# Kernel tuning notes

Measured on AMD Instinct MI355X. Metric: run time of the kernel, lower is better.

Reference implementation:

```python
import jax, jax.numpy as jnp
import numpy as np

N = 50000   # nodes
E = 800000  # edges
G = 64      # graphs in batch
H1, D1 = 2, 64   # gat1: 2 heads x 64
D2 = 32          # gat2: 1 head x 32
IN = 1
EPS = 1e-5


def _gat(h, src, dst, W, al, ar, Wres, bias, Hh, D):
    # DGL GATConv (eval mode): project, per-edge attention, edge softmax over dst, scatter-sum, residual + bias
    feat = (h @ W).reshape(N, Hh, D)                     # [N,H,D]
    el = jnp.sum(feat * al, axis=-1)                     # [N,H]
    er = jnp.sum(feat * ar, axis=-1)                     # [N,H]
    e = jax.nn.leaky_relu(el[src] + er[dst], 0.2)        # [E,H]
    m = jax.ops.segment_max(e, dst, num_segments=N)      # [N,H] (stable softmax)
    a = jnp.exp(e - m[dst])
    s = jax.ops.segment_sum(a, dst, num_segments=N)
    alpha = a / s[dst]                                   # [E,H]
    msg = feat[src] * alpha[:, :, None]                  # [E,H,D]
    rst = jax.ops.segment_sum(msg, dst, num_segments=N)  # [N,H,D]
    res = (h @ Wres).reshape(N, Hh, D)
    return rst + res + bias.reshape(1, Hh, D)


def _bn(x, gamma, beta, mean, var):
    return (x - mean) * jax.lax.rsqrt(var + EPS) * gamma + beta


def setup_inputs() -> dict:
    key = jax.random.key(0)
    ks = jax.random.split(key, 32)
    rn = lambda i, shape: jax.random.normal(ks[i], shape, jnp.float32) * 0.1
    inp = {
        'feat': jax.random.normal(ks[0], (N, IN), jnp.float32),
        'W1': rn(1, (IN, H1 * D1)), 'al1': rn(2, (H1, D1)), 'ar1': rn(3, (H1, D1)),
        'res1': rn(4, (IN, H1 * D1)), 'b1': rn(5, (H1 * D1,)),
        'g1_gamma': jnp.ones((H1 * D1,), jnp.float32), 'g1_beta': jnp.zeros((H1 * D1,), jnp.float32),
        'g1_mean': rn(6, (H1 * D1,)), 'g1_var': jax.random.uniform(ks[7], (H1 * D1,), jnp.float32) + 0.5,
        'W2': rn(8, (H1 * D1, D2)), 'al2': rn(9, (1, D2)), 'ar2': rn(10, (1, D2)),
        'res2': rn(11, (H1 * D1, D2)), 'b2': rn(12, (D2,)),
        'g2_gamma': jnp.ones((D2,), jnp.float32), 'g2_beta': jnp.zeros((D2,), jnp.float32),
        'g2_mean': rn(13, (D2,)), 'g2_var': jax.random.uniform(ks[14], (D2,), jnp.float32) + 0.5,
        'Wd1': rn(15, (D2, H1 * D1)), 'bd1': rn(16, (H1 * D1,)),
        'gd_gamma': jnp.ones((H1 * D1,), jnp.float32), 'gd_beta': jnp.zeros((H1 * D1,), jnp.float32),
        'gd_mean': rn(17, (H1 * D1,)), 'gd_var': jax.random.uniform(ks[18], (H1 * D1,), jnp.float32) + 0.5,
        'Wd2': rn(19, (H1 * D1, IN)), 'bd2': rn(20, (IN,)),
        'src': jax.random.randint(ks[21], (E,), 0, N, jnp.int32),
        'dst': jax.random.randint(ks[22], (E,), 0, N, jnp.int32),
        'graph_ids': jnp.sort(jax.random.randint(ks[23], (N,), 0, G, jnp.int32)),
    }
    return inp


def reference(feat, W1, al1, ar1, res1, b1, g1_gamma, g1_beta, g1_mean, g1_var,
              W2, al2, ar2, res2, b2, g2_gamma, g2_beta, g2_mean, g2_var,
              Wd1, bd1, gd_gamma, gd_beta, gd_mean, gd_var, Wd2, bd2,
              src, dst, graph_ids):
    h = _gat(feat, src, dst, W1, al1, ar1, res1, b1, H1, D1)   # [N,2,64]
    h = h.reshape(N, H1 * D1)
    h = jax.nn.relu(_bn(h, g1_gamma, g1_beta, g1_mean, g1_var))
    h = _gat(h, src, dst, W2, al2, ar2, res2, b2, 1, D2)       # [N,1,32]
    h = h.reshape(N, D2)
    h = jax.nn.relu(_bn(h, g2_gamma, g2_beta, g2_mean, g2_var))
    # dgl.mean_nodes over batched graphs
    counts = jax.ops.segment_sum(jnp.ones((N,), h.dtype), graph_ids, num_segments=G)
    graph_rep = jax.ops.segment_sum(h, graph_ids, num_segments=G) / jnp.maximum(counts, 1.0)[:, None]
    # decoder: Linear -> BN -> ReLU -> Linear (dropout off in eval)
    d = jax.nn.relu(_bn(h @ Wd1 + bd1, gd_gamma, gd_beta, gd_mean, gd_var))
    reconstruction = d @ Wd2 + bd2
    return graph_rep, reconstruction
```

## Files before the change

kernel.cpp:

```cpp
#include <hip/hip_runtime.h>
#include <hip/hip_bf16.h>

#define NN 50000
#define NE 800000
#define NG 64
#define C1 128
#define D2 32
#define NB 196
#define BN_EPS 1e-5f

#define CST_A   0
#define CST_B   2
#define CST_P   4
#define CST_Q   132
#define CST_R   260
#define CST_SC2 388
#define CST_RC2 420
#define CST_SD  452
#define CST_RD  580
#define CST_N   1024

#define UO_DEG   0
#define UO_CNT   50000
#define ZERO_UNITS 50004
#define UO_FLAG  50004
#define UO_LOC   50008
#define UO_BSUM  100008
#define UO_CARRY 100264
#define UO_ESRC  100520
#define UO_EOFF  500520
#define UO_FCAN  900520
#define UO_CST   950520
#define UO_F2    951544
#define UO_RS2   1751544
#define UO_EL2   3351544
#define UO_ER2   3401544
#define UO_END   3451544

__device__ __forceinline__ float lrelu(float x) { return fmaxf(x, 0.2f * x); }
__device__ __forceinline__ float bu2f(unsigned int u) {
    union { unsigned int i; float f; } v; v.i = (u & 0xFFFFu) << 16; return v.f;
}
__device__ __forceinline__ unsigned short f2bu(float f) {
    union { float f; unsigned int i; } v; v.f = f;
    unsigned int r = v.i + 0x7FFFu + ((v.i >> 16) & 1u);
    return (unsigned short)(r >> 16);
}
__device__ __forceinline__ float pk_lo(unsigned int w) {
    union { unsigned int i; float f; } v; v.i = w << 16; return v.f;
}
__device__ __forceinline__ float pk_hi(unsigned int w) {
    union { unsigned int i; float f; } v; v.i = w & 0xFFFF0000u; return v.f;
}
__device__ __forceinline__ float ldw(const void* p, int i, int bf) {
    return bf ? bu2f(((const unsigned short*)p)[i]) : ((const float*)p)[i];
}
__device__ __forceinline__ int offat(const int* loc, const int* carry, int i) {
    return loc[i] + carry[i >> 8];
}
__device__ __forceinline__ int sniff64(const unsigned int* fw, int l) {
    int cnt = 0;
    for (int j = l; j < 256; j += 64) {
        unsigned int b = (fw[j] >> 8) & 0x7Fu;
        cnt += (b >= 0x3Au && b <= 0x41u) ? 1 : 0;
    }
#pragma unroll
    for (int m = 32; m >= 1; m >>= 1) cnt += __shfl_xor(cnt, m);
    return (cnt > 128) ? 1 : 0;
}

__global__ void k_prep(const void* __restrict__ feat, const int* __restrict__ dst,
                       float* __restrict__ fcan, int* __restrict__ deg,
                       unsigned short* __restrict__ eoff,
                       const void* W1, const void* al1, const void* ar1,
                       const void* res1, const void* b1,
                       const void* g1g, const void* g1b, const void* g1m, const void* g1v,
                       const void* b2v, const void* g2g, const void* g2b,
                       const void* g2m, const void* g2v,
                       const void* bd1, const void* gdg, const void* gdb,
                       const void* gdm, const void* gdv,
                       int* __restrict__ flag, float* __restrict__ cst) {
    __shared__ int sBf;
    int t = threadIdx.x;
    if (t < 64) {
        int bf = sniff64((const unsigned int*)feat, t);
        if (t == 0) sBf = bf;
    }
    __syncthreads();
    int bf = sBf;

    if (blockIdx.x == 0) {
        if (t == 0) *flag = bf;
        if (t < 128) {
            if (t < 2) {
                float a = 0.0f, b = 0.0f;
                for (int d = 0; d < 64; ++d) {
                    float w = ldw(W1, t * 64 + d, bf);
                    a += w * ldw(al1, t * 64 + d, bf);
                    b += w * ldw(ar1, t * 64 + d, bf);
                }
                cst[CST_A + t] = a;
                cst[CST_B + t] = b;
            }
            {
                float sc = rsqrtf(ldw(g1v, t, bf) + BN_EPS) * ldw(g1g, t, bf);
                cst[CST_P + t] = ldw(W1, t, bf) * sc;
                cst[CST_Q + t] = ldw(res1, t, bf) * sc;
                cst[CST_R + t] = (ldw(b1, t, bf) - ldw(g1m, t, bf)) * sc + ldw(g1b, t, bf);
            }
            if (t < D2) {
                float sc = rsqrtf(ldw(g2v, t, bf) + BN_EPS) * ldw(g2g, t, bf);
                cst[CST_SC2 + t] = sc;
                cst[CST_RC2 + t] = (ldw(b2v, t, bf) - ldw(g2m, t, bf)) * sc + ldw(g2b, t, bf);
            }
            {
                float sc = rsqrtf(ldw(gdv, t, bf) + BN_EPS) * ldw(gdg, t, bf);
                cst[CST_SD + t] = sc;
                cst[CST_RD + t] = (ldw(bd1, t, bf) - ldw(gdm, t, bf)) * sc + ldw(gdb, t, bf);
            }
        }
    }

    int k = blockIdx.x * blockDim.x + t;
    if (k < NN) fcan[k] = ldw(feat, k, bf);
    if (k < NE) eoff[k] = (unsigned short)atomicAdd(&deg[dst[k]], 1);
}

__global__ __launch_bounds__(256) void k_scanA(const int* __restrict__ deg,
                                               int* __restrict__ loc,
                                               int* __restrict__ bsum,
                                               int* __restrict__ carry,
                                               int* __restrict__ cnt) {
    __shared__ int tmp[256];
    __shared__ int isLast;
    int t = threadIdx.x;
    int i = blockIdx.x * 256 + t;
    int v = (i < NN) ? deg[i] : 0;
    tmp[t] = v;
    __syncthreads();
    for (int off = 1; off < 256; off <<= 1) {
        int u = (t >= off) ? tmp[t - off] : 0;
        __syncthreads();
        tmp[t] += u;
        __syncthreads();
    }
    if (i < NN) loc[i] = tmp[t] - v;
    if (t == 255) {
        bsum[blockIdx.x] = tmp[255];
        __threadfence();
        int old = atomicAdd(cnt, 1);
        isLast = (old == NB - 1) ? 1 : 0;
    }
    __syncthreads();
    if (isLast) {
        __threadfence();
        int bv = (t < NB) ? bsum[t] : 0;
        tmp[t] = bv;
        __syncthreads();
        for (int off = 1; off < 256; off <<= 1) {
            int u = (t >= off) ? tmp[t - off] : 0;
            __syncthreads();
            tmp[t] += u;
            __syncthreads();
        }
        carry[t] = tmp[t] - bv;
    }
}

__global__ void k_fill(const int* __restrict__ src, const int* __restrict__ dst,
                       const int* __restrict__ loc, const int* __restrict__ carry,
                       const unsigned short* __restrict__ eoff,
                       unsigned short* __restrict__ esrc) {
    int k = blockIdx.x * blockDim.x + threadIdx.x;
    if (k >= NE) return;
    int d = dst[k];
    esrc[offat(loc, carry, d) + (int)eoff[k]] = (unsigned short)src[k];
}

__global__ __launch_bounds__(256) void k_layer1(
        const float* __restrict__ fcan, const void* W2, const void* res2,
        const void* al2, const void* ar2,
        const int* __restrict__ flag, const float* __restrict__ cst,
        const int* __restrict__ loc, const int* __restrict__ carry,
        const unsigned short* __restrict__ esrc,
        unsigned short* __restrict__ F2, float* __restrict__ RS2,
        float* __restrict__ EL2, float* __restrict__ ER2) {
    __shared__ unsigned int sW2pk[32 * 66];
    __shared__ unsigned int sR2pk[32 * 66];
    __shared__ unsigned int sH1pk[32 * 66];
    __shared__ float sP[C1], sQ[C1], sR[C1];
    __shared__ float sAl[D2], sAr[D2];
    int t = threadIdx.x;
    int bf = *flag;
    for (int u = t; u < 2048; u += 256) {
        int cw = u >> 5, l2 = u & 31;
        unsigned int wlo = (unsigned int)f2bu(ldw(W2, cw * D2 + l2, bf));
        unsigned int whi = (unsigned int)f2bu(ldw(W2, (cw + 64) * D2 + l2, bf));
        sW2pk[l2 * 66 + cw] = wlo | (whi << 16);
        unsigned int rlo = (unsigned int)f2bu(ldw(res2, cw * D2 + l2, bf));
        unsigned int rhi = (unsigned int)f2bu(ldw(res2, (cw + 64) * D2 + l2, bf));
        sR2pk[l2 * 66 + cw] = rlo | (rhi << 16);
    }
    if (t < C1) { sP[t] = cst[CST_P + t]; sQ[t] = cst[CST_Q + t]; sR[t] = cst[CST_R + t]; }
    if (t < D2) { sAl[t] = ldw(al2, t, bf); sAr[t] = ldw(ar2, t, bf); }
    __syncthreads();

    int l = t & 31;
    int g = t >> 5;
    int base = blockIdx.x * 32;
    float A0 = cst[CST_A + 0], A1 = cst[CST_A + 1];
    float B0 = cst[CST_B + 0], B1 = cst[CST_B + 1];

    int e0k[4], e1k[4];
    float fiK[4];
#pragma unroll
    for (int k = 0; k < 4; ++k) {
        int i = base + g * 4 + k;
        if (i < NN) {
            e0k[k] = offat(loc, carry, i);
            e1k[k] = (i + 1 < NN) ? offat(loc, carry, i + 1) : NE;
            fiK[k] = fcan[i];
        } else { e0k[k] = 0; e1k[k] = 0; fiK[k] = 0.0f; }
    }
    float S0[4], S1[4], N0[4], N1[4];
#pragma unroll
    for (int k = 0; k < 4; ++k) { S0[k] = S1[k] = N0[k] = N1[k] = 0.0f; }
    int sA[4];
#pragma unroll
    for (int k = 0; k < 4; ++k) sA[k] = (e0k[k] + l < e1k[k]) ? (int)esrc[e0k[k] + l] : 0;
    float fA[4];
#pragma unroll
    for (int k = 0; k < 4; ++k) fA[k] = fcan[sA[k]];
#pragma unroll
    for (int k = 0; k < 4; ++k) {
        if (e0k[k] + l < e1k[k]) {
            float w0 = __expf(lrelu(A0 * fA[k] + B0 * fiK[k]));
            float w1 = __expf(lrelu(A1 * fA[k] + B1 * fiK[k]));
            S0[k] += w0; N0[k] += w0 * fA[k];
            S1[k] += w1; N1[k] += w1 * fA[k];
        }
    }
#pragma unroll
    for (int k = 0; k < 4; ++k) {
        for (int e = e0k[k] + l + 32; e < e1k[k]; e += 32) {
            int s = (int)esrc[e];
            float fs = fcan[s];
            float w0 = __expf(lrelu(A0 * fs + B0 * fiK[k]));
            float w1 = __expf(lrelu(A1 * fs + B1 * fiK[k]));
            S0[k] += w0; N0[k] += w0 * fs;
            S1[k] += w1; N1[k] += w1 * fs;
        }
    }
#pragma unroll
    for (int m = 16; m >= 1; m >>= 1) {
#pragma unroll
        for (int k = 0; k < 4; ++k) {
            S0[k] += __shfl_xor(S0[k], m); N0[k] += __shfl_xor(N0[k], m);
            S1[k] += __shfl_xor(S1[k], m); N1[k] += __shfl_xor(N1[k], m);
        }
    }
#pragma unroll
    for (int k = 0; k < 4; ++k) {
        int slot = g * 4 + k;
        float T0 = S0[k] > 0.0f ? N0[k] / S0[k] : 0.0f;
        float T1 = S1[k] > 0.0f ? N1[k] / S1[k] : 0.0f;
        float h0  = fmaxf(sP[l]      * T0 + sQ[l]      * fiK[k] + sR[l],      0.0f);
        float h1v = fmaxf(sP[l + 32] * T0 + sQ[l + 32] * fiK[k] + sR[l + 32], 0.0f);
        float h2v = fmaxf(sP[l + 64] * T1 + sQ[l + 64] * fiK[k] + sR[l + 64], 0.0f);
        float h3v = fmaxf(sP[l + 96] * T1 + sQ[l + 96] * fiK[k] + sR[l + 96], 0.0f);
        sH1pk[slot * 66 + l]      = (unsigned int)f2bu(h0)  | ((unsigned int)f2bu(h2v) << 16);
        sH1pk[slot * 66 + l + 32] = (unsigned int)f2bu(h1v) | ((unsigned int)f2bu(h3v) << 16);
    }
    __syncthreads();

    int w = t >> 6;
    int half = (t >> 5) & 1;
    int nb0 = w * 8 + half * 4;
    float aF[4] = {0.f, 0.f, 0.f, 0.f}, aR[4] = {0.f, 0.f, 0.f, 0.f};
    for (int cw = 0; cw < 64; cw += 2) {
        uint2 wq = *(const uint2*)&sW2pk[l * 66 + cw];
        uint2 rq = *(const uint2*)&sR2pk[l * 66 + cw];
        float w_a = pk_lo(wq.x), w_b = pk_hi(wq.x), w_c = pk_lo(wq.y), w_d = pk_hi(wq.y);
        float r_a = pk_lo(rq.x), r_b = pk_hi(rq.x), r_c = pk_lo(rq.y), r_d = pk_hi(rq.y);
#pragma unroll
        for (int n = 0; n < 4; ++n) {
            uint2 hq = *(const uint2*)&sH1pk[(nb0 + n) * 66 + cw];
            float h_a = pk_lo(hq.x), h_b = pk_hi(hq.x), h_c = pk_lo(hq.y), h_d = pk_hi(hq.y);
            aF[n] = fmaf(h_a, w_a, fmaf(h_b, w_b, fmaf(h_c, w_c, fmaf(h_d, w_d, aF[n]))));
            aR[n] = fmaf(h_a, r_a, fmaf(h_b, r_b, fmaf(h_c, r_c, fmaf(h_d, r_d, aR[n]))));
        }
    }
#pragma unroll
    for (int n = 0; n < 4; ++n) {
        int i = base + nb0 + n;
        if (i < NN) {
            float elp = aF[n] * sAl[l], erp = aF[n] * sAr[l];
#pragma unroll
            for (int m = 16; m >= 1; m >>= 1) {
                elp += __shfl_xor(elp, m);
                erp += __shfl_xor(erp, m);
            }
            if (l == 0) { EL2[i] = elp; ER2[i] = erp; }
            F2[(size_t)i * D2 + l]  = f2bu(aF[n]);
            RS2[(size_t)i * D2 + l] = aR[n];
        }
    }
}

__global__ __launch_bounds__(256) void k_final(
        const void* Wd1, const void* Wd2, const void* bd2,
        const int* __restrict__ flag, const float* __restrict__ cst,
        const int* __restrict__ loc, const int* __restrict__ carry,
        const unsigned short* __restrict__ esrc,
        const unsigned short* __restrict__ F2, float* __restrict__ RS2,
        const float* __restrict__ EL2, const float* __restrict__ ER2,
        float* __restrict__ out) {
    __shared__ float sWd1[C1 * D2];
    __shared__ float sWd2[C1];
    __shared__ float sSd[C1], sRd[C1];
    __shared__ float sSc2[D2], sRc2[D2];
    __shared__ float sH2[8 * D2];
    int t = threadIdx.x;
    int bf = *flag;
    for (int u = t; u < C1 * D2; u += 256) sWd1[u] = ldw(Wd1, u, bf);
    for (int u = t; u < C1; u += 256) {
        sWd2[u] = ldw(Wd2, u, bf);
        sSd[u] = cst[CST_SD + u]; sRd[u] = cst[CST_RD + u];
    }
    if (t < D2) { sSc2[t] = cst[CST_SC2 + t]; sRc2[t] = cst[CST_RC2 + t]; }
    __syncthreads();

    int i = (blockIdx.x * 256 + t) >> 5;
    int l = t & 31;
    int nb = t >> 5;

    float eri = ER2[i];
    int e0 = offat(loc, carry, i);
    int e1 = (i + 1 < NN) ? offat(loc, carry, i + 1) : NE;
    float aF0 = 0.0f, aF1 = 0.0f, aF2 = 0.0f, aF3 = 0.0f;
    float S0 = 0.0f, S1 = 0.0f, S2 = 0.0f, S3 = 0.0f;
    int e = e0;
    for (; e < e1 && (e & 3); ++e) {
        int sA = (int)esrc[e];
        float wA = __expf(lrelu(EL2[sA] + eri));
        S0 += wA;
        aF0 = fmaf(wA, bu2f(F2[(size_t)sA * D2 + l]), aF0);
    }
    for (; e + 3 < e1; e += 4) {
        ushort4 q = *(const ushort4*)&esrc[e];
        int sA = q.x, sB = q.y, sC = q.z, sD = q.w;
        float wA = __expf(lrelu(EL2[sA] + eri));
        float wB = __expf(lrelu(EL2[sB] + eri));
        float wC = __expf(lrelu(EL2[sC] + eri));
        float wD = __expf(lrelu(EL2[sD] + eri));
        float vA = bu2f(F2[(size_t)sA * D2 + l]);
        float vB = bu2f(F2[(size_t)sB * D2 + l]);
        float vC = bu2f(F2[(size_t)sC * D2 + l]);
        float vD = bu2f(F2[(size_t)sD * D2 + l]);
        S0 += wA; S1 += wB; S2 += wC; S3 += wD;
        aF0 = fmaf(wA, vA, aF0);
        aF1 = fmaf(wB, vB, aF1);
        aF2 = fmaf(wC, vC, aF2);
        aF3 = fmaf(wD, vD, aF3);
    }
    for (; e < e1; ++e) {
        int sA = (int)esrc[e];
        float wA = __expf(lrelu(EL2[sA] + eri));
        S0 += wA;
        aF0 = fmaf(wA, bu2f(F2[(size_t)sA * D2 + l]), aF0);
    }
    float S = (S0 + S1) + (S2 + S3);
    float aF = (aF0 + aF1) + (aF2 + aF3);
    float inv = S > 0.0f ? 1.0f / S : 0.0f;

    float h2 = fmaxf((aF * inv + RS2[(size_t)i * D2 + l]) * sSc2[l] + sRc2[l], 0.0f);
    RS2[(size_t)i * D2 + l] = h2;

    sH2[nb * D2 + l] = h2;
    float ac0 = 0.0f, ac1 = 0.0f, ac2 = 0.0f, ac3 = 0.0f;
#pragma unroll
    for (int d = 0; d < D2; ++d) {
        float h = sH2[nb * D2 + d];
        const float* wr = &sWd1[d * C1 + l];
        ac0 = fmaf(h, wr[0],  ac0);
        ac1 = fmaf(h, wr[32], ac1);
        ac2 = fmaf(h, wr[64], ac2);
        ac3 = fmaf(h, wr[96], ac3);
    }
    float rec = fmaxf(ac0 * sSd[l]      + sRd[l],      0.0f) * sWd2[l]
              + fmaxf(ac1 * sSd[l + 32] + sRd[l + 32], 0.0f) * sWd2[l + 32]
              + fmaxf(ac2 * sSd[l + 64] + sRd[l + 64], 0.0f) * sWd2[l + 64]
              + fmaxf(ac3 * sSd[l + 96] + sRd[l + 96], 0.0f) * sWd2[l + 96];
#pragma unroll
    for (int m = 16; m >= 1; m >>= 1) rec += __shfl_xor(rec, m);
    if (l == 0) out[NG * D2 + i] = rec + ldw(bd2, 0, bf);
}

__global__ __launch_bounds__(256) void k_pool2(const int* __restrict__ gid,
                                               const float* __restrict__ H2,
                                               float* __restrict__ out) {
    __shared__ int sLo, sHi;
    __shared__ float sAcc[8 * D2];
    int g = blockIdx.x;
    int t = threadIdx.x;
    if (t == 0) {
        int lo = 0, hi = NN;
        while (lo < hi) { int m = (lo + hi) >> 1; if (gid[m] < g) lo = m + 1; else hi = m; }
        sLo = lo;
        lo = 0; hi = NN;
        while (lo < hi) { int m = (lo + hi) >> 1; if (gid[m] < g + 1) lo = m + 1; else hi = m; }
        sHi = lo;
    }
    __syncthreads();
    int lo = sLo, hi = sHi;
    int l = t & 31, row = t >> 5;
    float acc = 0.0f;
    for (int i = lo + row; i < hi; i += 8)
        acc += H2[(size_t)i * D2 + l];
    sAcc[row * D2 + l] = acc;
    __syncthreads();
    if (row == 0) {
#pragma unroll
        for (int r = 1; r < 8; ++r) acc += sAcc[r * D2 + l];
        float c = (float)(hi - lo);
        out[g * D2 + l] = acc / fmaxf(c, 1.0f);
    }
}

extern "C" void kernel_launch(void* const* d_in, const int* in_sizes, int n_in,
                              void* d_out, int out_size, void* d_ws, size_t ws_size,
                              hipStream_t stream) {
    const void* feat = d_in[0];
    const void* W1 = d_in[1];  const void* al1 = d_in[2];  const void* ar1 = d_in[3];
    const void* res1 = d_in[4]; const void* b1 = d_in[5];
    const void* g1g = d_in[6]; const void* g1b = d_in[7];
    const void* g1m = d_in[8]; const void* g1v = d_in[9];
    const void* W2 = d_in[10]; const void* al2 = d_in[11]; const void* ar2 = d_in[12];
    const void* res2 = d_in[13]; const void* b2v = d_in[14];
    const void* g2g = d_in[15]; const void* g2b = d_in[16];
    const void* g2m = d_in[17]; const void* g2v = d_in[18];
    const void* Wd1 = d_in[19]; const void* bd1 = d_in[20];
    const void* gdg = d_in[21]; const void* gdb = d_in[22];
    const void* gdm = d_in[23]; const void* gdv = d_in[24];
    const void* Wd2 = d_in[25]; const void* bd2 = d_in[26];
    const int* src = (const int*)d_in[27];
    const int* dst = (const int*)d_in[28];
    const int* gid = (const int*)d_in[29];

    unsigned int* wsu = (unsigned int*)d_ws;
    int* deg    = (int*)(wsu + UO_DEG);
    int* cnt    = (int*)(wsu + UO_CNT);
    int* flag   = (int*)(wsu + UO_FLAG);
    int* loc    = (int*)(wsu + UO_LOC);
    int* bsum   = (int*)(wsu + UO_BSUM);
    int* carry  = (int*)(wsu + UO_CARRY);
    unsigned short* esrc = (unsigned short*)(wsu + UO_ESRC);
    unsigned short* eoff = (unsigned short*)(wsu + UO_EOFF);
    float* fcan = (float*)(wsu + UO_FCAN);
    float* cst  = (float*)(wsu + UO_CST);
    unsigned short* F2 = (unsigned short*)(wsu + UO_F2);
    float* RS2  = (float*)(wsu + UO_RS2);
    float* EL2  = (float*)(wsu + UO_EL2);
    float* ER2  = (float*)(wsu + UO_ER2);

    hipMemsetAsync(d_ws, 0, (size_t)ZERO_UNITS * 4, stream);

    k_prep<<<(NE + 255) / 256, 256, 0, stream>>>(feat, dst, fcan, deg, eoff,
                                                 W1, al1, ar1, res1, b1,
                                                 g1g, g1b, g1m, g1v,
                                                 b2v, g2g, g2b, g2m, g2v,
                                                 bd1, gdg, gdb, gdm, gdv,
                                                 flag, cst);
    k_scanA<<<NB, 256, 0, stream>>>(deg, loc, bsum, carry, cnt);
    k_fill<<<(NE + 255) / 256, 256, 0, stream>>>(src, dst, loc, carry, eoff, esrc);

    k_layer1<<<(NN + 31) / 32, 256, 0, stream>>>(fcan, W2, res2, al2, ar2, flag, cst,
                                                 loc, carry, esrc, F2, RS2, EL2, ER2);

    k_final<<<(NN * 32) / 256, 256, 0, stream>>>(Wd1, Wd2, bd2, flag, cst,
                                                 loc, carry, esrc, F2, RS2, EL2, ER2,
                                                 (float*)d_out);

    k_pool2<<<NG, 256, 0, stream>>>(gid, RS2, (float*)d_out);
}
```

Measured before the change: 294.8 us.

## Replace CSR scan/fill with fixed-capacity per-node edge slots plus overflow list

Builds the dst-grouped adjacency directly in the atomic-count kernel by writing each edge into a fixed 32-slot row per destination node, with edges beyond 32 appended to a global overflow list. This removes the prefix-scan and fill kernels and two launches. In exchange, nodes with degree above 32 must linearly scan the whole overflow list in both aggregation kernels, and the padded slot array uses more memory. With average degree 16, a Poisson-like tail gives some overflow, so scan cost depends on how many overflow edges there are.

```diff
diff --git a/kernel.cpp b/kernel.cpp
--- a/kernel.cpp
+++ b/kernel.cpp
@@ -6,7 +6,7 @@
 #define NG 64
 #define C1 128
 #define D2 32
-#define NB 196
+#define CAP 32
 #define BN_EPS 1e-5f
 
 #define CST_A   0
@@ -21,21 +21,18 @@
 #define CST_N   1024
 
 #define UO_DEG   0
-#define UO_CNT   50000
+#define UO_OVFC  50000
 #define ZERO_UNITS 50004
 #define UO_FLAG  50004
-#define UO_LOC   50008
-#define UO_BSUM  100008
-#define UO_CARRY 100264
-#define UO_ESRC  100520
-#define UO_EOFF  500520
-#define UO_FCAN  900520
-#define UO_CST   950520
-#define UO_F2    951544
-#define UO_RS2   1751544
-#define UO_EL2   3351544
-#define UO_ER2   3401544
-#define UO_END   3451544
+#define UO_CST   50008
+#define UO_ESRC2 51040
+#define UO_OVF   851040
+#define UO_FCAN  2451040
+#define UO_F2    2501040
+#define UO_RS2   3301040
+#define UO_EL2   4901040
+#define UO_ER2   4951040
+#define UO_END   5001040
 
 __device__ __forceinline__ float lrelu(float x) { return fmaxf(x, 0.2f * x); }
 __device__ __forceinline__ float bu2f(unsigned int u) {
@@ -54,9 +51,6 @@
 }
 __device__ __forceinline__ float ldw(const void* p, int i, int bf) {
     return bf ? bu2f(((const unsigned short*)p)[i]) : ((const float*)p)[i];
-}
-__device__ __forceinline__ int offat(const int* loc, const int* carry, int i) {
-    return loc[i] + carry[i >> 8];
 }
 __device__ __forceinline__ int sniff64(const unsigned int* fw, int l) {
     int cnt = 0;
@@ -70,8 +64,10 @@
 }
 
 __global__ void k_prep(const void* __restrict__ feat, const int* __restrict__ dst,
+                       const int* __restrict__ src,
                        float* __restrict__ fcan, int* __restrict__ deg,
-                       unsigned short* __restrict__ eoff,
+                       unsigned short* __restrict__ esrc2,
+                       int2* __restrict__ ovf, int* __restrict__ ovfc,
                        const void* W1, const void* al1, const void* ar1,
                        const void* res1, const void* b1,
                        const void* g1g, const void* g1b, const void* g1m, const void* g1v,
@@ -123,66 +119,24 @@
 
     int k = blockIdx.x * blockDim.x + t;
     if (k < NN) fcan[k] = ldw(feat, k, bf);
-    if (k < NE) eoff[k] = (unsigned short)atomicAdd(&deg[dst[k]], 1);
-}
-
-__global__ __launch_bounds__(256) void k_scanA(const int* __restrict__ deg,
-                                               int* __restrict__ loc,
-                                               int* __restrict__ bsum,
-                                               int* __restrict__ carry,
-                                               int* __restrict__ cnt) {
-    __shared__ int tmp[256];
-    __shared__ int isLast;
-    int t = threadIdx.x;
-    int i = blockIdx.x * 256 + t;
-    int v = (i < NN) ? deg[i] : 0;
-    tmp[t] = v;
-    __syncthreads();
-    for (int off = 1; off < 256; off <<= 1) {
-        int u = (t >= off) ? tmp[t - off] : 0;
-        __syncthreads();
-        tmp[t] += u;
-        __syncthreads();
-    }
-    if (i < NN) loc[i] = tmp[t] - v;
-    if (t == 255) {
-        bsum[blockIdx.x] = tmp[255];
-        __threadfence();
-        int old = atomicAdd(cnt, 1);
-        isLast = (old == NB - 1) ? 1 : 0;
-    }
-    __syncthreads();
-    if (isLast) {
-        __threadfence();
-        int bv = (t < NB) ? bsum[t] : 0;
-        tmp[t] = bv;
-        __syncthreads();
-        for (int off = 1; off < 256; off <<= 1) {
-            int u = (t >= off) ? tmp[t - off] : 0;
-            __syncthreads();
-            tmp[t] += u;
-            __syncthreads();
-        }
-        carry[t] = tmp[t] - bv;
-    }
-}
-
-__global__ void k_fill(const int* __restrict__ src, const int* __restrict__ dst,
-                       const int* __restrict__ loc, const int* __restrict__ carry,
-                       const unsigned short* __restrict__ eoff,
-                       unsigned short* __restrict__ esrc) {
-    int k = blockIdx.x * blockDim.x + threadIdx.x;
-    if (k >= NE) return;
-    int d = dst[k];
-    esrc[offat(loc, carry, d) + (int)eoff[k]] = (unsigned short)src[k];
+    if (k < NE) {
+        int d = dst[k];
+        int slot = atomicAdd(&deg[d], 1);
+        if (slot < CAP) {
+            esrc2[d * CAP + slot] = (unsigned short)src[k];
+        } else {
+            int p = atomicAdd(ovfc, 1);
+            ovf[p] = make_int2(d, src[k]);
+        }
+    }
 }
 
 __global__ __launch_bounds__(256) void k_layer1(
         const float* __restrict__ fcan, const void* W2, const void* res2,
         const void* al2, const void* ar2,
         const int* __restrict__ flag, const float* __restrict__ cst,
-        const int* __restrict__ loc, const int* __restrict__ carry,
-        const unsigned short* __restrict__ esrc,
+        const int* __restrict__ deg, const unsigned short* __restrict__ esrc2,
+        const int2* __restrict__ ovf, const int* __restrict__ ovfc,
         unsigned short* __restrict__ F2, float* __restrict__ RS2,
         float* __restrict__ EL2, float* __restrict__ ER2) {
     __shared__ unsigned int sW2pk[32 * 66];
@@ -211,29 +165,30 @@
     float A0 = cst[CST_A + 0], A1 = cst[CST_A + 1];
     float B0 = cst[CST_B + 0], B1 = cst[CST_B + 1];
 
-    int e0k[4], e1k[4];
+    int dcap[4], draw[4];
     float fiK[4];
 #pragma unroll
     for (int k = 0; k < 4; ++k) {
         int i = base + g * 4 + k;
         if (i < NN) {
-            e0k[k] = offat(loc, carry, i);
-            e1k[k] = (i + 1 < NN) ? offat(loc, carry, i + 1) : NE;
+            draw[k] = deg[i];
+            dcap[k] = draw[k] < CAP ? draw[k] : CAP;
             fiK[k] = fcan[i];
-        } else { e0k[k] = 0; e1k[k] = 0; fiK[k] = 0.0f; }
+        } else { draw[k] = 0; dcap[k] = 0; fiK[k] = 0.0f; }
     }
     float S0[4], S1[4], N0[4], N1[4];
 #pragma unroll
     for (int k = 0; k < 4; ++k) { S0[k] = S1[k] = N0[k] = N1[k] = 0.0f; }
     int sA[4];
 #pragma unroll
-    for (int k = 0; k < 4; ++k) sA[k] = (e0k[k] + l < e1k[k]) ? (int)esrc[e0k[k] + l] : 0;
+    for (int k = 0; k < 4; ++k)
+        sA[k] = (l < dcap[k]) ? (int)esrc2[(base + g * 4 + k) * CAP + l] : 0;
     float fA[4];
 #pragma unroll
     for (int k = 0; k < 4; ++k) fA[k] = fcan[sA[k]];
 #pragma unroll
     for (int k = 0; k < 4; ++k) {
-        if (e0k[k] + l < e1k[k]) {
+        if (l < dcap[k]) {
             float w0 = __expf(lrelu(A0 * fA[k] + B0 * fiK[k]));
             float w1 = __expf(lrelu(A1 * fA[k] + B1 * fiK[k]));
             S0[k] += w0; N0[k] += w0 * fA[k];
@@ -242,13 +197,19 @@
     }
 #pragma unroll
     for (int k = 0; k < 4; ++k) {
-        for (int e = e0k[k] + l + 32; e < e1k[k]; e += 32) {
-            int s = (int)esrc[e];
-            float fs = fcan[s];
-            float w0 = __expf(lrelu(A0 * fs + B0 * fiK[k]));
-            float w1 = __expf(lrelu(A1 * fs + B1 * fiK[k]));
-            S0[k] += w0; N0[k] += w0 * fs;
-            S1[k] += w1; N1[k] += w1 * fs;
+        if (draw[k] > CAP) {
+            int i = base + g * 4 + k;
+            int novf = *ovfc;
+            for (int p = l; p < novf; p += 32) {
+                int2 o = ovf[p];
+                if (o.x == i) {
+                    float fs = fcan[o.y];
+                    float w0 = __expf(lrelu(A0 * fs + B0 * fiK[k]));
+                    float w1 = __expf(lrelu(A1 * fs + B1 * fiK[k]));
+                    S0[k] += w0; N0[k] += w0 * fs;
+                    S1[k] += w1; N1[k] += w1 * fs;
+                }
+            }
         }
     }
 #pragma unroll
@@ -310,8 +271,8 @@
 __global__ __launch_bounds__(256) void k_final(
         const void* Wd1, const void* Wd2, const void* bd2,
         const int* __restrict__ flag, const float* __restrict__ cst,
-        const int* __restrict__ loc, const int* __restrict__ carry,
-        const unsigned short* __restrict__ esrc,
+        const int* __restrict__ deg, const unsigned short* __restrict__ esrc2,
+        const int2* __restrict__ ovf, const int* __restrict__ ovfc,
         const unsigned short* __restrict__ F2, float* __restrict__ RS2,
         const float* __restrict__ EL2, const float* __restrict__ ER2,
         float* __restrict__ out) {
@@ -335,19 +296,14 @@
     int nb = t >> 5;
 
     float eri = ER2[i];
-    int e0 = offat(loc, carry, i);
-    int e1 = (i + 1 < NN) ? offat(loc, carry, i + 1) : NE;
+    int dr = deg[i];
+    int dcap = dr < CAP ? dr : CAP;
+    const unsigned short* row = &esrc2[i * CAP];
     float aF0 = 0.0f, aF1 = 0.0f, aF2 = 0.0f, aF3 = 0.0f;
     float S0 = 0.0f, S1 = 0.0f, S2 = 0.0f, S3 = 0.0f;
-    int e = e0;
-    for (; e < e1 && (e & 3); ++e) {
-        int sA = (int)esrc[e];
-        float wA = __expf(lrelu(EL2[sA] + eri));
-        S0 += wA;
-        aF0 = fmaf(wA, bu2f(F2[(size_t)sA * D2 + l]), aF0);
-    }
-    for (; e + 3 < e1; e += 4) {
-        ushort4 q = *(const ushort4*)&esrc[e];
+    int j = 0;
+    for (; j + 3 < dcap; j += 4) {
+        ushort4 q = *(const ushort4*)&row[j];
         int sA = q.x, sB = q.y, sC = q.z, sD = q.w;
         float wA = __expf(lrelu(EL2[sA] + eri));
         float wB = __expf(lrelu(EL2[sB] + eri));
@@ -363,11 +319,22 @@
         aF2 = fmaf(wC, vC, aF2);
         aF3 = fmaf(wD, vD, aF3);
     }
-    for (; e < e1; ++e) {
-        int sA = (int)esrc[e];
+    for (; j < dcap; ++j) {
+        int sA = (int)row[j];
         float wA = __expf(lrelu(EL2[sA] + eri));
         S0 += wA;
         aF0 = fmaf(wA, bu2f(F2[(size_t)sA * D2 + l]), aF0);
+    }
+    if (dr > CAP) {
+        int novf = *ovfc;
+        for (int p = 0; p < novf; ++p) {
+            int2 o = ovf[p];
+            if (o.x == i) {
+                float wA = __expf(lrelu(EL2[o.y] + eri));
+                S0 += wA;
+                aF0 = fmaf(wA, bu2f(F2[(size_t)o.y * D2 + l]), aF0);
+            }
+        }
     }
     float S = (S0 + S1) + (S2 + S3);
     float aF = (aF0 + aF1) + (aF2 + aF3);
@@ -449,15 +416,12 @@
 
     unsigned int* wsu = (unsigned int*)d_ws;
     int* deg    = (int*)(wsu + UO_DEG);
-    int* cnt    = (int*)(wsu + UO_CNT);
+    int* ovfc   = (int*)(wsu + UO_OVFC);
     int* flag   = (int*)(wsu + UO_FLAG);
-    int* loc    = (int*)(wsu + UO_LOC);
-    int* bsum   = (int*)(wsu + UO_BSUM);
-    int* carry  = (int*)(wsu + UO_CARRY);
-    unsigned short* esrc = (unsigned short*)(wsu + UO_ESRC);
-    unsigned short* eoff = (unsigned short*)(wsu + UO_EOFF);
+    float* cst  = (float*)(wsu + UO_CST);
+    unsigned short* esrc2 = (unsigned short*)(wsu + UO_ESRC2);
+    int2* ovf   = (int2*)(wsu + UO_OVF);
     float* fcan = (float*)(wsu + UO_FCAN);
-    float* cst  = (float*)(wsu + UO_CST);
     unsigned short* F2 = (unsigned short*)(wsu + UO_F2);
     float* RS2  = (float*)(wsu + UO_RS2);
     float* EL2  = (float*)(wsu + UO_EL2);
@@ -465,20 +429,21 @@
 
     hipMemsetAsync(d_ws, 0, (size_t)ZERO_UNITS * 4, stream);
 
-    k_prep<<<(NE + 255) / 256, 256, 0, stream>>>(feat, dst, fcan, deg, eoff,
+    k_prep<<<(NE + 255) / 256, 256, 0, stream>>>(feat, dst, src, fcan, deg,
+                                                 esrc2, ovf, ovfc,
                                                  W1, al1, ar1, res1, b1,
                                                  g1g, g1b, g1m, g1v,
                                                  b2v, g2g, g2b, g2m, g2v,
                                                  bd1, gdg, gdb, gdm, gdv,
                                                  flag, cst);
-    k_scanA<<<NB, 256, 0, stream>>>(deg, loc, bsum, carry, cnt);
-    k_fill<<<(NE + 255) / 256, 256, 0, stream>>>(src, dst, loc, carry, eoff, esrc);
 
     k_layer1<<<(NN + 31) / 32, 256, 0, stream>>>(fcan, W2, res2, al2, ar2, flag, cst,
-                                                 loc, carry, esrc, F2, RS2, EL2, ER2);
+                                                 deg, esrc2, ovf, ovfc,
+                                                 F2, RS2, EL2, ER2);
 
     k_final<<<(NN * 32) / 256, 256, 0, stream>>>(Wd1, Wd2, bd2, flag, cst,
-                                                 loc, carry, esrc, F2, RS2, EL2, ER2,
+                                                 deg, esrc2, ovf, ovfc,
+                                                 F2, RS2, EL2, ER2,
                                                  (float*)d_out);
 
     k_pool2<<<NG, 256, 0, stream>>>(gid, RS2, (float*)d_out);
```

New measurement: 276.0 us. 1.07x faster.
